# Kernel tuning notes

Measured on AMD Instinct MI355X. Metric: run time of the kernel, lower is better.

Reference implementation:

```python
import jax, jax.numpy as jnp
import numpy as np

B, C, W, H = 32, 512, 28, 28  # input spatial = 2*init_width x 2*init_height
HEADS = 8


def setup_inputs() -> dict:
    key = jax.random.key(0)
    ks = jax.random.split(key, 9)
    d = C // HEADS
    s = 0.05
    return {
        "x": jax.random.normal(ks[0], (B, C, W, H), jnp.float32),
        # 1x1 conv weights == dense [out_c, in_c] + bias
        "wq": jax.random.normal(ks[1], (C, C), jnp.float32) * s,
        "bq": jax.random.normal(ks[2], (C,), jnp.float32) * s,
        "wk": jax.random.normal(ks[3], (C, C), jnp.float32) * s,
        "bk": jax.random.normal(ks[4], (C,), jnp.float32) * s,
        "wv": jax.random.normal(ks[5], (C, C), jnp.float32) * s,
        "bv": jax.random.normal(ks[6], (C,), jnp.float32) * s,
        "rel_h": jax.random.normal(ks[7], (1, HEADS, d, 1, H), jnp.float32),
        "rel_w": jax.random.normal(ks[8], (1, HEADS, d, W, 1), jnp.float32),
    }


def reference(x, wq, bq, wk, bk, wv, bv, rel_h, rel_w):
    b, c, w, h = x.shape
    heads = rel_h.shape[1]
    d = c // heads
    n = w * h

    def proj(wt, bi):
        # 1x1 conv == per-pixel dense over channels
        y = jnp.einsum('oc,bcwh->bowh', wt, x) + bi[None, :, None, None]
        return y.reshape(b, heads, d, n)  # [B, H, d, N]

    q = proj(wq, bq)
    k = proj(wk, bk)
    v = proj(wv, bv)

    # content-content: q^T k -> [B, H, N, N]
    cc = jnp.einsum('bhdn,bhdm->bhnm', q, k)
    # relative position bias: (rel_h + rel_w) broadcast to [H, d, 2w0*2h0] = [H, d, N]
    pos = (rel_h + rel_w).reshape(heads, d, n)
    # content-position: pos^T @ q -> [B, H, N, N]
    cp = jnp.einsum('hdp,bhdn->bhpn', pos, q)

    attn = jax.nn.softmax(cc + cp, axis=-1)  # softmax over last dim
    # out = v @ attn^T : [B, H, d, N]
    out = jnp.einsum('bhdn,bhmn->bhdm', v, attn)
    return out.reshape(b, c, w, h)
```

## Files before the change

kernel.cpp:

```cpp
#include <hip/hip_runtime.h>


#define BATCH 32
#define CCH   512
#define NHEAD 8
#define DH    64
#define NTOK  784
#define WSP   28
#define OT    128
#define NT    160
#define NXB   5
#define NJT   10
#define WLD   40
#define CH    64
#define NCHUNK 13
#define NIBLK  7
#define KQLD  136
#define VLD   72

typedef unsigned short u16;
typedef unsigned int   u32;
typedef short  short8  __attribute__((ext_vector_type(8)));
typedef float  floatx4 __attribute__((ext_vector_type(4)));

__device__ __forceinline__ u16 f2bf(float f) {
    union { float f; u32 i; } v; v.f = f;
    u32 x = v.i;
    return (u16)((x + 0x7FFFu + ((x >> 16) & 1u)) >> 16);
}
__device__ __forceinline__ u32 f2u(float f) { union { float f; u32 i; } v; v.f = f; return v.i; }
__device__ __forceinline__ float u2f(u32 u) { union { u32 i; float f; } v; v.i = u; return v.f; }

__device__ __forceinline__ u32 packsplit(float f) {
    const u32 hib = f2u(f) & 0xFFFF0000u;
    const float lo = f - u2f(hib);
    return ((u32)f2bf(lo) << 16) | (hib >> 16);
}

__global__ __launch_bounds__(256)
void pack_weights(const float* __restrict__ wq, const float* __restrict__ wk,
                  const float* __restrict__ wv,
                  u32* __restrict__ Wqp, u32* __restrict__ Wkp, u32* __restrict__ Wvp)
{
    const int i = blockIdx.x * 256 + threadIdx.x;
    if (i < CCH * CCH) {
        Wqp[i] = packsplit(wq[i]);
        Wkp[i] = packsplit(wk[i]);
        Wvp[i] = packsplit(wv[i]);
    }
}

__global__ __launch_bounds__(256)
void pack_xt(const float* __restrict__ x, u32* __restrict__ Xt, int b0)
{
    const int bl = blockIdx.z;
    const int c0 = blockIdx.y * 32;
    const int n0 = blockIdx.x * 32;
    const int t  = threadIdx.x;
    const int tn = t & 31;
    const int tr = t >> 5;

    __shared__ float tile[32][33];

    const size_t xb = (size_t)(b0 + bl) * CCH * NTOK;
    #pragma unroll
    for (int k = 0; k < 4; k++) {
        const int c = tr + k * 8;
        const int n = n0 + tn;
        if (n < NTOK)
            tile[c][tn] = x[xb + (size_t)(c0 + c) * NTOK + n];
    }
    __syncthreads();
    const size_t ob = (size_t)bl * NTOK * CCH;
    #pragma unroll
    for (int k = 0; k < 4; k++) {
        const int n = n0 + tr + k * 8;
        const int c = c0 + tn;
        if (n < NTOK)
            Xt[ob + (size_t)n * CCH + c] = packsplit(tile[tn][tr + k * 8]);
    }
}

__global__ __launch_bounds__(512, 4)
void qkv_proj(const u32* __restrict__ Xt,
              const u32* __restrict__ Wqp, const float* __restrict__ bq,
              const u32* __restrict__ Wkp, const float* __restrict__ bk,
              const u32* __restrict__ Wvp, const float* __restrict__ bv,
              u32* __restrict__ Qp, u32* __restrict__ Kp, u16* __restrict__ Vo,
              int nbatch)
{
    const int t    = threadIdx.x;
    const int lane = t & 63;
    const int wid  = t >> 6;
    const int z    = blockIdx.z;
    const int proj = z / nbatch;
    const int bl   = z - proj * nbatch;
    const int o0   = blockIdx.y * OT;
    int n0 = blockIdx.x * NT;
    if (n0 > NTOK - NT) n0 = NTOK - NT;

    const u32*   Wp   = (proj == 0) ? Wqp : (proj == 1) ? Wkp : Wvp;
    const float* bias = (proj == 0) ? bq  : (proj == 1) ? bk  : bv;
    const bool   isV  = (proj == 2);

    __shared__ u16 wh[OT][WLD], wl[OT][WLD];
    __shared__ u16 xh[NT][WLD], xl[NT][WLD];

    const int m    = lane & 15;
    const int quad = lane >> 4;

    floatx4 acc[NJT];
    #pragma unroll
    for (int j = 0; j < NJT; j++) acc[j] = (floatx4){0.f, 0.f, 0.f, 0.f};

    const int wo = t >> 2;
    const int wc = (t & 3) * 8;
    const int xrow = t >> 2;
    const int xc8  = (t & 3) * 8;
    const int xrow2 = 128 + (t >> 2);

    const size_t xtbase = (size_t)bl * NTOK * CCH;

    uint4 wv0, wv1, xv0, xv1, xv2, xv3;
    {
        wv0 = *reinterpret_cast<const uint4*>(&Wp[(size_t)(o0 + wo) * CCH + 0 + wc]);
        wv1 = *reinterpret_cast<const uint4*>(&Wp[(size_t)(o0 + wo) * CCH + 0 + wc + 4]);
        xv0 = *reinterpret_cast<const uint4*>(&Xt[xtbase + (size_t)(n0 + xrow) * CCH + 0 + xc8]);
        xv1 = *reinterpret_cast<const uint4*>(&Xt[xtbase + (size_t)(n0 + xrow) * CCH + 0 + xc8 + 4]);
        if (t < 128) {
            xv2 = *reinterpret_cast<const uint4*>(&Xt[xtbase + (size_t)(n0 + xrow2) * CCH + 0 + xc8]);
            xv3 = *reinterpret_cast<const uint4*>(&Xt[xtbase + (size_t)(n0 + xrow2) * CCH + 0 + xc8 + 4]);
        }
    }

    for (int c0 = 0; c0 < CCH; c0 += 32) {
        __syncthreads();
        {
            const u32 wr[8] = {wv0.x, wv0.y, wv0.z, wv0.w, wv1.x, wv1.y, wv1.z, wv1.w};
            ushort4 h0 = make_ushort4((u16)(wr[0] & 0xFFFF), (u16)(wr[1] & 0xFFFF), (u16)(wr[2] & 0xFFFF), (u16)(wr[3] & 0xFFFF));
            ushort4 h1 = make_ushort4((u16)(wr[4] & 0xFFFF), (u16)(wr[5] & 0xFFFF), (u16)(wr[6] & 0xFFFF), (u16)(wr[7] & 0xFFFF));
            *reinterpret_cast<ushort4*>(&wh[wo][wc])     = h0;
            *reinterpret_cast<ushort4*>(&wh[wo][wc + 4]) = h1;
            if (!isV) {
                ushort4 l0 = make_ushort4((u16)(wr[0] >> 16), (u16)(wr[1] >> 16), (u16)(wr[2] >> 16), (u16)(wr[3] >> 16));
                ushort4 l1 = make_ushort4((u16)(wr[4] >> 16), (u16)(wr[5] >> 16), (u16)(wr[6] >> 16), (u16)(wr[7] >> 16));
                *reinterpret_cast<ushort4*>(&wl[wo][wc])     = l0;
                *reinterpret_cast<ushort4*>(&wl[wo][wc + 4]) = l1;
            }
        }
        {
            const u32 xr[8] = {xv0.x, xv0.y, xv0.z, xv0.w, xv1.x, xv1.y, xv1.z, xv1.w};
            ushort4 h0 = make_ushort4((u16)(xr[0] & 0xFFFF), (u16)(xr[1] & 0xFFFF), (u16)(xr[2] & 0xFFFF), (u16)(xr[3] & 0xFFFF));
            ushort4 h1 = make_ushort4((u16)(xr[4] & 0xFFFF), (u16)(xr[5] & 0xFFFF), (u16)(xr[6] & 0xFFFF), (u16)(xr[7] & 0xFFFF));
            ushort4 l0 = make_ushort4((u16)(xr[0] >> 16), (u16)(xr[1] >> 16), (u16)(xr[2] >> 16), (u16)(xr[3] >> 16));
            ushort4 l1 = make_ushort4((u16)(xr[4] >> 16), (u16)(xr[5] >> 16), (u16)(xr[6] >> 16), (u16)(xr[7] >> 16));
            *reinterpret_cast<ushort4*>(&xh[xrow][xc8])     = h0;
            *reinterpret_cast<ushort4*>(&xh[xrow][xc8 + 4]) = h1;
            *reinterpret_cast<ushort4*>(&xl[xrow][xc8])     = l0;
            *reinterpret_cast<ushort4*>(&xl[xrow][xc8 + 4]) = l1;
        }
        if (t < 128) {
            const u32 xr[8] = {xv2.x, xv2.y, xv2.z, xv2.w, xv3.x, xv3.y, xv3.z, xv3.w};
            ushort4 h0 = make_ushort4((u16)(xr[0] & 0xFFFF), (u16)(xr[1] & 0xFFFF), (u16)(xr[2] & 0xFFFF), (u16)(xr[3] & 0xFFFF));
            ushort4 h1 = make_ushort4((u16)(xr[4] & 0xFFFF), (u16)(xr[5] & 0xFFFF), (u16)(xr[6] & 0xFFFF), (u16)(xr[7] & 0xFFFF));
            ushort4 l0 = make_ushort4((u16)(xr[0] >> 16), (u16)(xr[1] >> 16), (u16)(xr[2] >> 16), (u16)(xr[3] >> 16));
            ushort4 l1 = make_ushort4((u16)(xr[4] >> 16), (u16)(xr[5] >> 16), (u16)(xr[6] >> 16), (u16)(xr[7] >> 16));
            *reinterpret_cast<ushort4*>(&xh[xrow2][xc8])     = h0;
            *reinterpret_cast<ushort4*>(&xh[xrow2][xc8 + 4]) = h1;
            *reinterpret_cast<ushort4*>(&xl[xrow2][xc8])     = l0;
            *reinterpret_cast<ushort4*>(&xl[xrow2][xc8 + 4]) = l1;
        }
        __syncthreads();

        if (c0 + 32 < CCH) {
            wv0 = *reinterpret_cast<const uint4*>(&Wp[(size_t)(o0 + wo) * CCH + c0 + 32 + wc]);
            wv1 = *reinterpret_cast<const uint4*>(&Wp[(size_t)(o0 + wo) * CCH + c0 + 32 + wc + 4]);
            xv0 = *reinterpret_cast<const uint4*>(&Xt[xtbase + (size_t)(n0 + xrow) * CCH + c0 + 32 + xc8]);
            xv1 = *reinterpret_cast<const uint4*>(&Xt[xtbase + (size_t)(n0 + xrow) * CCH + c0 + 32 + xc8 + 4]);
            if (t < 128) {
                xv2 = *reinterpret_cast<const uint4*>(&Xt[xtbase + (size_t)(n0 + xrow2) * CCH + c0 + 32 + xc8]);
                xv3 = *reinterpret_cast<const uint4*>(&Xt[xtbase + (size_t)(n0 + xrow2) * CCH + c0 + 32 + xc8 + 4]);
            }
        }
        __builtin_amdgcn_sched_barrier(0);

        const short8 Ah = *reinterpret_cast<const short8*>(&wh[wid * 16 + m][quad * 8]);
        short8 Al{};
        if (!isV) Al = *reinterpret_cast<const short8*>(&wl[wid * 16 + m][quad * 8]);
        #pragma unroll
        for (int jt = 0; jt < NJT; jt++) {
            const short8 Bh = *reinterpret_cast<const short8*>(&xh[jt * 16 + m][quad * 8]);
            const short8 Bl = *reinterpret_cast<const short8*>(&xl[jt * 16 + m][quad * 8]);
            acc[jt] = __builtin_amdgcn_mfma_f32_16x16x32_bf16(Ah, Bh, acc[jt], 0, 0, 0);
            acc[jt] = __builtin_amdgcn_mfma_f32_16x16x32_bf16(Ah, Bl, acc[jt], 0, 0, 0);
            if (!isV)
                acc[jt] = __builtin_amdgcn_mfma_f32_16x16x32_bf16(Al, Bh, acc[jt], 0, 0, 0);
        }
    }

    const size_t obase = (size_t)bl * CCH * NTOK;
    #pragma unroll
    for (int r = 0; r < 4; r++) {
        const int o = o0 + wid * 16 + quad * 4 + r;
        const float bi = bias[o];
        #pragma unroll
        for (int jt = 0; jt < NJT; jt++) {
            const int n = n0 + jt * 16 + m;
            const float val = acc[jt][r] + bi;
            const size_t idx = obase + (size_t)o * NTOK + n;
            if (proj == 0)      Qp[idx] = packsplit(val);
            else if (proj == 1) Kp[idx] = packsplit(val);
            else                Vo[idx] = f2bf(val);
        }
    }
}

__global__ __launch_bounds__(512)
void attn_kernel(const u32* __restrict__ Qp, const u32* __restrict__ Kp,
                 const u16* __restrict__ V,
                 const float* __restrict__ rel_h, const float* __restrict__ rel_w,
                 float* __restrict__ out, int b0)
{
    const int t    = threadIdx.x;
    const int lane = t & 63;
    const int wid  = t >> 6;
    const int m    = lane & 15;
    const int quad = lane >> 4;
    const int bl   = blockIdx.x;
    const int h    = blockIdx.y;
    int i0 = blockIdx.z * 128;
    if (i0 > NTOK - 128) i0 = NTOK - 128;
    const int b  = b0 + bl;
    const int hd = h * DH;
    const size_t base  = ((size_t)bl * CCH + hd) * NTOK;
    const size_t baseo = ((size_t)b  * CCH + hd) * NTOK;

    __shared__ u16 kqh[CH][KQLD];
    __shared__ u16 kql[CH][KQLD];
    __shared__ u16 vt[DH][VLD];
    __shared__ u16 pt[128][VLD];

    short8 Bh[4], Bl[4];
    {
        const int ig = i0 + wid * 16 + m;
        const int iw = ig / WSP, ih = ig % WSP;
        #pragma unroll
        for (int c = 0; c < 4; c++) {
            union { short8 v; u16 u[8]; } hb, lb;
            #pragma unroll
            for (int idx = 0; idx < 8; idx++) {
                const int k = c * 32 + quad * 8 + idx;
                if (k < DH) {
                    const u32 p = Qp[base + (size_t)k * NTOK + ig];
                    hb.u[idx] = (u16)(p & 0xFFFFu);
                    lb.u[idx] = (u16)(p >> 16);
                } else {
                    const int d = k - DH;
                    const float pos = rel_h[(size_t)(hd + d) * WSP + ih]
                                    + rel_w[(size_t)(hd + d) * WSP + iw];
                    const u32 hib = f2u(pos) & 0xFFFF0000u;
                    hb.u[idx] = (u16)(hib >> 16);
                    lb.u[idx] = f2bf(pos - u2f(hib));
                }
            }
            Bh[c] = hb.v; Bl[c] = lb.v;
        }
    }

    floatx4 Oacc[4];
    #pragma unroll
    for (int dt = 0; dt < 4; dt++) Oacc[dt] = (floatx4){0.f, 0.f, 0.f, 0.f};
    float mrun = -1e30f, lrun = 0.f;

    const int cg4 = (t & 31) * 4;
    const int jb4 = (t >> 5) * 4;
    const int vd  = t >> 3;
    const int vj  = (t & 7) * 8;

    for (int chn = 0; chn < NCHUNK; chn++) {
        const int j0 = chn * CH;
        __syncthreads();

        {
            u32 kv[4][4];
            #pragma unroll
            for (int cc = 0; cc < 4; cc++) {
                const int c = cg4 + cc;
                const u32* src = (c < DH) ? (Kp + base + (size_t)c * NTOK)
                                          : (Qp + base + (size_t)(c - DH) * NTOK);
                const uint4 a = *reinterpret_cast<const uint4*>(&src[j0 + jb4]);
                kv[cc][0] = a.x; kv[cc][1] = a.y; kv[cc][2] = a.z; kv[cc][3] = a.w;
            }
            #pragma unroll
            for (int jj = 0; jj < 4; jj++) {
                const ushort4 hi = make_ushort4((u16)(kv[0][jj] & 0xFFFFu), (u16)(kv[1][jj] & 0xFFFFu),
                                                (u16)(kv[2][jj] & 0xFFFFu), (u16)(kv[3][jj] & 0xFFFFu));
                const ushort4 lo = make_ushort4((u16)(kv[0][jj] >> 16), (u16)(kv[1][jj] >> 16),
                                                (u16)(kv[2][jj] >> 16), (u16)(kv[3][jj] >> 16));
                *reinterpret_cast<ushort4*>(&kqh[jb4 + jj][cg4]) = hi;
                *reinterpret_cast<ushort4*>(&kql[jb4 + jj][cg4]) = lo;
            }
        }
        if (j0 + vj + 8 <= NTOK) {
            const uint4 a = *reinterpret_cast<const uint4*>(&V[base + (size_t)vd * NTOK + j0 + vj]);
            *reinterpret_cast<uint4*>(&vt[vd][vj]) = a;
        } else {
            #pragma unroll
            for (int u = 0; u < 8; u++)
                vt[vd][vj + u] = (j0 + vj + u < NTOK) ? V[base + (size_t)vd * NTOK + j0 + vj + u] : (u16)0;
        }
        __syncthreads();

        floatx4 Sacc[4];
        #pragma unroll
        for (int js = 0; js < 4; js++) Sacc[js] = (floatx4){0.f, 0.f, 0.f, 0.f};
        #pragma unroll
        for (int c = 0; c < 4; c++) {
            #pragma unroll
            for (int js = 0; js < 4; js++) {
                const short8 Ah = *reinterpret_cast<const short8*>(&kqh[js * 16 + m][c * 32 + quad * 8]);
                const short8 Al = *reinterpret_cast<const short8*>(&kql[js * 16 + m][c * 32 + quad * 8]);
                Sacc[js] = __builtin_amdgcn_mfma_f32_16x16x32_bf16(Ah, Bh[c], Sacc[js], 0, 0, 0);
                Sacc[js] = __builtin_amdgcn_mfma_f32_16x16x32_bf16(Ah, Bl[c], Sacc[js], 0, 0, 0);
                Sacc[js] = __builtin_amdgcn_mfma_f32_16x16x32_bf16(Al, Bh[c], Sacc[js], 0, 0, 0);
            }
        }

        float sv[16];
        #pragma unroll
        for (int js = 0; js < 4; js++)
            #pragma unroll
            for (int r = 0; r < 4; r++) sv[js * 4 + r] = Sacc[js][r];
        if (j0 + CH > NTOK) {
            #pragma unroll
            for (int js = 0; js < 4; js++)
                #pragma unroll
                for (int r = 0; r < 4; r++)
                    if (j0 + js * 16 + quad * 4 + r >= NTOK) sv[js * 4 + r] = -1e30f;
        }
        float mc = sv[0];
        #pragma unroll
        for (int u = 1; u < 16; u++) mc = fmaxf(mc, sv[u]);
        mc = fmaxf(mc, __shfl_xor(mc, 16, 64));
        mc = fmaxf(mc, __shfl_xor(mc, 32, 64));
        const float mnew  = fmaxf(mrun, mc);
        const float alpha = __expf(mrun - mnew);
        float ps = 0.f;
        #pragma unroll
        for (int u = 0; u < 16; u++) {
            const float p = __expf(sv[u] - mnew);
            sv[u] = p;
            ps += p;
        }
        ps += __shfl_xor(ps, 16, 64);
        ps += __shfl_xor(ps, 32, 64);
        lrun = lrun * alpha + ps;
        mrun = mnew;
        #pragma unroll
        for (int dt = 0; dt < 4; dt++)
            #pragma unroll
            for (int r = 0; r < 4; r++) Oacc[dt][r] *= alpha;

        #pragma unroll
        for (int js = 0; js < 4; js++) {
            const ushort4 pw = make_ushort4(f2bf(sv[js * 4 + 0]), f2bf(sv[js * 4 + 1]),
                                            f2bf(sv[js * 4 + 2]), f2bf(sv[js * 4 + 3]));
            *reinterpret_cast<ushort4*>(&pt[wid * 16 + m][js * 16 + quad * 4]) = pw;
        }

        #pragma unroll
        for (int joff = 0; joff < CH; joff += 32) {
            const short8 Bp = *reinterpret_cast<const short8*>(&pt[wid * 16 + m][joff + quad * 8]);
            #pragma unroll
            for (int dt = 0; dt < 4; dt++) {
                const short8 Av = *reinterpret_cast<const short8*>(&vt[dt * 16 + m][joff + quad * 8]);
                Oacc[dt] = __builtin_amdgcn_mfma_f32_16x16x32_bf16(Av, Bp, Oacc[dt], 0, 0, 0);
            }
        }
    }

    const float linv = 1.f / lrun;
    #pragma unroll
    for (int dt = 0; dt < 4; dt++) {
        #pragma unroll
        for (int r = 0; r < 4; r++) {
            const int d = dt * 16 + quad * 4 + r;
            out[baseo + (size_t)d * NTOK + i0 + wid * 16 + m] = Oacc[dt][r] * linv;
        }
    }
}

extern "C" void kernel_launch(void* const* d_in, const int* in_sizes, int n_in,
                              void* d_out, int out_size, void* d_ws, size_t ws_size,
                              hipStream_t stream)
{
    const float* x  = (const float*)d_in[0];
    const float* wq = (const float*)d_in[1];
    const float* bq = (const float*)d_in[2];
    const float* wk = (const float*)d_in[3];
    const float* bk = (const float*)d_in[4];
    const float* wv = (const float*)d_in[5];
    const float* bv = (const float*)d_in[6];
    const float* rh = (const float*)d_in[7];
    const float* rw = (const float*)d_in[8];
    float* out = (float*)d_out;

    const size_t perB = (size_t)CCH * NTOK;
    const size_t WELEM = (size_t)CCH * CCH;
    const size_t weightBytes = 3 * WELEM * 4;
    const size_t perBatchBytes = perB * 14;

    size_t avail = (ws_size > weightBytes) ? (ws_size - weightBytes) : perBatchBytes;
    size_t nb_s = avail / perBatchBytes;
    int nb = (int)(nb_s < 1 ? 1 : (nb_s > BATCH ? BATCH : nb_s));

    u32* Wqp = (u32*)d_ws;
    u32* Wkp = Wqp + WELEM;
    u32* Wvp = Wkp + WELEM;
    u32* chunk0 = Wvp + WELEM;

    pack_weights<<<dim3((CCH * CCH + 255) / 256), dim3(256), 0, stream>>>(wq, wk, wv, Wqp, Wkp, Wvp);

    for (int b0 = 0; b0 < BATCH; b0 += nb) {
        const int curb = (BATCH - b0 < nb) ? (BATCH - b0) : nb;
        u32* Xt = chunk0;
        u32* Qp = Xt + (size_t)curb * perB;
        u32* Kp = Qp + (size_t)curb * perB;
        u16* Vb = (u16*)(Kp + (size_t)curb * perB);

        dim3 gx((NTOK + 31) / 32, CCH / 32, curb);
        pack_xt<<<gx, dim3(256), 0, stream>>>(x, Xt, b0);

        dim3 gp(NXB, CCH / OT, 3 * curb);
        qkv_proj<<<gp, dim3(512), 0, stream>>>(Xt, Wqp, bq, Wkp, bk, Wvp, bv,
                                               Qp, Kp, Vb, curb);

        dim3 ga(curb, NHEAD, NIBLK);
        attn_kernel<<<ga, dim3(512), 0, stream>>>(Qp, Kp, Vb, rh, rw, out, b0);
    }
}
```

Measured before the change: 494.4 us.

## Process two query row tiles per wave in attention kernel with 256 threads

Halves the attention block to 4 waves, with each wave handling 32 query rows as two 16-row subtiles. Each K/Q fragment and V fragment read from LDS now feeds two MFMA streams, which cuts LDS traffic per MFMA. The global-to-LDS staging loop is widened so fewer threads still fill the same tiles. The cost is more registers per thread (doubled accumulators and B fragments), fewer threads to hide load latency, and launch bounds that ask for two blocks per CU.

```diff
diff --git a/kernel.cpp b/kernel.cpp
--- a/kernel.cpp
+++ b/kernel.cpp
@@ -215,7 +215,7 @@
     }
 }
 
-__global__ __launch_bounds__(512)
+__global__ __launch_bounds__(256, 2)
 void attn_kernel(const u32* __restrict__ Qp, const u32* __restrict__ Kp,
                  const u16* __restrict__ V,
                  const float* __restrict__ rel_h, const float* __restrict__ rel_w,
@@ -240,9 +240,10 @@
     __shared__ u16 vt[DH][VLD];
     __shared__ u16 pt[128][VLD];
 
-    short8 Bh[4], Bl[4];
-    {
-        const int ig = i0 + wid * 16 + m;
+    short8 Bh[2][4], Bl[2][4];
+    #pragma unroll
+    for (int s = 0; s < 2; s++) {
+        const int ig = i0 + wid * 32 + s * 16 + m;
         const int iw = ig / WSP, ih = ig % WSP;
         #pragma unroll
         for (int c = 0; c < 4; c++) {
@@ -263,129 +264,151 @@
                     lb.u[idx] = f2bf(pos - u2f(hib));
                 }
             }
-            Bh[c] = hb.v; Bl[c] = lb.v;
-        }
-    }
-
-    floatx4 Oacc[4];
-    #pragma unroll
-    for (int dt = 0; dt < 4; dt++) Oacc[dt] = (floatx4){0.f, 0.f, 0.f, 0.f};
-    float mrun = -1e30f, lrun = 0.f;
+            Bh[s][c] = hb.v; Bl[s][c] = lb.v;
+        }
+    }
+
+    floatx4 Oacc[2][4];
+    #pragma unroll
+    for (int s = 0; s < 2; s++)
+        #pragma unroll
+        for (int dt = 0; dt < 4; dt++) Oacc[s][dt] = (floatx4){0.f, 0.f, 0.f, 0.f};
+    float mrun[2] = {-1e30f, -1e30f}, lrun[2] = {0.f, 0.f};
 
     const int cg4 = (t & 31) * 4;
-    const int jb4 = (t >> 5) * 4;
-    const int vd  = t >> 3;
-    const int vj  = (t & 7) * 8;
+    const int jb8 = (t >> 5) * 8;
+    const int vd  = t >> 2;
+    const int vj  = (t & 3) * 16;
 
     for (int chn = 0; chn < NCHUNK; chn++) {
         const int j0 = chn * CH;
         __syncthreads();
 
         {
-            u32 kv[4][4];
+            u32 kv[4][8];
             #pragma unroll
             for (int cc = 0; cc < 4; cc++) {
                 const int c = cg4 + cc;
                 const u32* src = (c < DH) ? (Kp + base + (size_t)c * NTOK)
                                           : (Qp + base + (size_t)(c - DH) * NTOK);
-                const uint4 a = *reinterpret_cast<const uint4*>(&src[j0 + jb4]);
-                kv[cc][0] = a.x; kv[cc][1] = a.y; kv[cc][2] = a.z; kv[cc][3] = a.w;
-            }
-            #pragma unroll
-            for (int jj = 0; jj < 4; jj++) {
+                const uint4 a = *reinterpret_cast<const uint4*>(&src[j0 + jb8]);
+                const uint4 bq4 = *reinterpret_cast<const uint4*>(&src[j0 + jb8 + 4]);
+                kv[cc][0] = a.x;   kv[cc][1] = a.y;   kv[cc][2] = a.z;   kv[cc][3] = a.w;
+                kv[cc][4] = bq4.x; kv[cc][5] = bq4.y; kv[cc][6] = bq4.z; kv[cc][7] = bq4.w;
+            }
+            #pragma unroll
+            for (int jj = 0; jj < 8; jj++) {
                 const ushort4 hi = make_ushort4((u16)(kv[0][jj] & 0xFFFFu), (u16)(kv[1][jj] & 0xFFFFu),
                                                 (u16)(kv[2][jj] & 0xFFFFu), (u16)(kv[3][jj] & 0xFFFFu));
                 const ushort4 lo = make_ushort4((u16)(kv[0][jj] >> 16), (u16)(kv[1][jj] >> 16),
                                                 (u16)(kv[2][jj] >> 16), (u16)(kv[3][jj] >> 16));
-                *reinterpret_cast<ushort4*>(&kqh[jb4 + jj][cg4]) = hi;
-                *reinterpret_cast<ushort4*>(&kql[jb4 + jj][cg4]) = lo;
-            }
-        }
-        if (j0 + vj + 8 <= NTOK) {
+                *reinterpret_cast<ushort4*>(&kqh[jb8 + jj][cg4]) = hi;
+                *reinterpret_cast<ushort4*>(&kql[jb8 + jj][cg4]) = lo;
+            }
+        }
+        if (j0 + vj + 16 <= NTOK) {
             const uint4 a = *reinterpret_cast<const uint4*>(&V[base + (size_t)vd * NTOK + j0 + vj]);
-            *reinterpret_cast<uint4*>(&vt[vd][vj]) = a;
+            const uint4 c = *reinterpret_cast<const uint4*>(&V[base + (size_t)vd * NTOK + j0 + vj + 8]);
+            *reinterpret_cast<uint4*>(&vt[vd][vj])     = a;
+            *reinterpret_cast<uint4*>(&vt[vd][vj + 8]) = c;
         } else {
             #pragma unroll
-            for (int u = 0; u < 8; u++)
+            for (int u = 0; u < 16; u++)
                 vt[vd][vj + u] = (j0 + vj + u < NTOK) ? V[base + (size_t)vd * NTOK + j0 + vj + u] : (u16)0;
         }
         __syncthreads();
 
-        floatx4 Sacc[4];
-        #pragma unroll
-        for (int js = 0; js < 4; js++) Sacc[js] = (floatx4){0.f, 0.f, 0.f, 0.f};
+        floatx4 Sacc[2][4];
+        #pragma unroll
+        for (int s = 0; s < 2; s++)
+            #pragma unroll
+            for (int js = 0; js < 4; js++) Sacc[s][js] = (floatx4){0.f, 0.f, 0.f, 0.f};
         #pragma unroll
         for (int c = 0; c < 4; c++) {
             #pragma unroll
             for (int js = 0; js < 4; js++) {
                 const short8 Ah = *reinterpret_cast<const short8*>(&kqh[js * 16 + m][c * 32 + quad * 8]);
                 const short8 Al = *reinterpret_cast<const short8*>(&kql[js * 16 + m][c * 32 + quad * 8]);
-                Sacc[js] = __builtin_amdgcn_mfma_f32_16x16x32_bf16(Ah, Bh[c], Sacc[js], 0, 0, 0);
-                Sacc[js] = __builtin_amdgcn_mfma_f32_16x16x32_bf16(Ah, Bl[c], Sacc[js], 0, 0, 0);
-                Sacc[js] = __builtin_amdgcn_mfma_f32_16x16x32_bf16(Al, Bh[c], Sacc[js], 0, 0, 0);
-            }
-        }
-
-        float sv[16];
-        #pragma unroll
-        for (int js = 0; js < 4; js++)
-            #pragma unroll
-            for (int r = 0; r < 4; r++) sv[js * 4 + r] = Sacc[js][r];
-        if (j0 + CH > NTOK) {
+                #pragma unroll
+                for (int s = 0; s < 2; s++) {
+                    Sacc[s][js] = __builtin_amdgcn_mfma_f32_16x16x32_bf16(Ah, Bh[s][c], Sacc[s][js], 0, 0, 0);
+                    Sacc[s][js] = __builtin_amdgcn_mfma_f32_16x16x32_bf16(Ah, Bl[s][c], Sacc[s][js], 0, 0, 0);
+                    Sacc[s][js] = __builtin_amdgcn_mfma_f32_16x16x32_bf16(Al, Bh[s][c], Sacc[s][js], 0, 0, 0);
+                }
+            }
+        }
+
+        #pragma unroll
+        for (int s = 0; s < 2; s++) {
+            float sv[16];
             #pragma unroll
             for (int js = 0; js < 4; js++)
                 #pragma unroll
-                for (int r = 0; r < 4; r++)
-                    if (j0 + js * 16 + quad * 4 + r >= NTOK) sv[js * 4 + r] = -1e30f;
-        }
-        float mc = sv[0];
-        #pragma unroll
-        for (int u = 1; u < 16; u++) mc = fmaxf(mc, sv[u]);
-        mc = fmaxf(mc, __shfl_xor(mc, 16, 64));
-        mc = fmaxf(mc, __shfl_xor(mc, 32, 64));
-        const float mnew  = fmaxf(mrun, mc);
-        const float alpha = __expf(mrun - mnew);
-        float ps = 0.f;
-        #pragma unroll
-        for (int u = 0; u < 16; u++) {
-            const float p = __expf(sv[u] - mnew);
-            sv[u] = p;
-            ps += p;
-        }
-        ps += __shfl_xor(ps, 16, 64);
-        ps += __shfl_xor(ps, 32, 64);
-        lrun = lrun * alpha + ps;
-        mrun = mnew;
-        #pragma unroll
-        for (int dt = 0; dt < 4; dt++)
-            #pragma unroll
-            for (int r = 0; r < 4; r++) Oacc[dt][r] *= alpha;
-
-        #pragma unroll
-        for (int js = 0; js < 4; js++) {
-            const ushort4 pw = make_ushort4(f2bf(sv[js * 4 + 0]), f2bf(sv[js * 4 + 1]),
-                                            f2bf(sv[js * 4 + 2]), f2bf(sv[js * 4 + 3]));
-            *reinterpret_cast<ushort4*>(&pt[wid * 16 + m][js * 16 + quad * 4]) = pw;
+                for (int r = 0; r < 4; r++) sv[js * 4 + r] = Sacc[s][js][r];
+            if (j0 + CH > NTOK) {
+                #pragma unroll
+                for (int js = 0; js < 4; js++)
+                    #pragma unroll
+                    for (int r = 0; r < 4; r++)
+                        if (j0 + js * 16 + quad * 4 + r >= NTOK) sv[js * 4 + r] = -1e30f;
+            }
+            float mc = sv[0];
+            #pragma unroll
+            for (int u = 1; u < 16; u++) mc = fmaxf(mc, sv[u]);
+            mc = fmaxf(mc, __shfl_xor(mc, 16, 64));
+            mc = fmaxf(mc, __shfl_xor(mc, 32, 64));
+            const float mnew  = fmaxf(mrun[s], mc);
+            const float alpha = __expf(mrun[s] - mnew);
+            float ps = 0.f;
+            #pragma unroll
+            for (int u = 0; u < 16; u++) {
+                const float p = __expf(sv[u] - mnew);
+                sv[u] = p;
+                ps += p;
+            }
+            ps += __shfl_xor(ps, 16, 64);
+            ps += __shfl_xor(ps, 32, 64);
+            lrun[s] = lrun[s] * alpha + ps;
+            mrun[s] = mnew;
+            #pragma unroll
+            for (int dt = 0; dt < 4; dt++)
+                #pragma unroll
+                for (int r = 0; r < 4; r++) Oacc[s][dt][r] *= alpha;
+
+            #pragma unroll
+            for (int js = 0; js < 4; js++) {
+                const ushort4 pw = make_ushort4(f2bf(sv[js * 4 + 0]), f2bf(sv[js * 4 + 1]),
+                                                f2bf(sv[js * 4 + 2]), f2bf(sv[js * 4 + 3]));
+                *reinterpret_cast<ushort4*>(&pt[wid * 32 + s * 16 + m][js * 16 + quad * 4]) = pw;
+            }
         }
 
         #pragma unroll
         for (int joff = 0; joff < CH; joff += 32) {
-            const short8 Bp = *reinterpret_cast<const short8*>(&pt[wid * 16 + m][joff + quad * 8]);
-            #pragma unroll
-            for (int dt = 0; dt < 4; dt++) {
-                const short8 Av = *reinterpret_cast<const short8*>(&vt[dt * 16 + m][joff + quad * 8]);
-                Oacc[dt] = __builtin_amdgcn_mfma_f32_16x16x32_bf16(Av, Bp, Oacc[dt], 0, 0, 0);
-            }
-        }
-    }
-
-    const float linv = 1.f / lrun;
-    #pragma unroll
-    for (int dt = 0; dt < 4; dt++) {
-        #pragma unroll
-        for (int r = 0; r < 4; r++) {
-            const int d = dt * 16 + quad * 4 + r;
-            out[baseo + (size_t)d * NTOK + i0 + wid * 16 + m] = Oacc[dt][r] * linv;
+            short8 Av[4];
+            #pragma unroll
+            for (int dt = 0; dt < 4; dt++)
+                Av[dt] = *reinterpret_cast<const short8*>(&vt[dt * 16 + m][joff + quad * 8]);
+            #pragma unroll
+            for (int s = 0; s < 2; s++) {
+                const short8 Bp = *reinterpret_cast<const short8*>(&pt[wid * 32 + s * 16 + m][joff + quad * 8]);
+                #pragma unroll
+                for (int dt = 0; dt < 4; dt++)
+                    Oacc[s][dt] = __builtin_amdgcn_mfma_f32_16x16x32_bf16(Av[dt], Bp, Oacc[s][dt], 0, 0, 0);
+            }
+        }
+    }
+
+    #pragma unroll
+    for (int s = 0; s < 2; s++) {
+        const float linv = 1.f / lrun[s];
+        #pragma unroll
+        for (int dt = 0; dt < 4; dt++) {
+            #pragma unroll
+            for (int r = 0; r < 4; r++) {
+                const int d = dt * 16 + quad * 4 + r;
+                out[baseo + (size_t)d * NTOK + i0 + wid * 32 + s * 16 + m] = Oacc[s][dt][r] * linv;
+            }
         }
     }
 }
@@ -436,6 +459,6 @@
                                                Qp, Kp, Vb, curb);
 
         dim3 ga(curb, NHEAD, NIBLK);
-        attn_kernel<<<ga, dim3(512), 0, stream>>>(Qp, Kp, Vb, rh, rw, out, b0);
-    }
-}
+        attn_kernel<<<ga, dim3(256), 0, stream>>>(Qp, Kp, Vb, rh, rw, out, b0);
+    }
+}
```

After: 514.7 us. 4.1% more time.
